# Kernel optimization log

Measured on AMD Instinct MI355X. Metric: run time of the kernel, lower is better.

## Reference

```python
import jax, jax.numpy as jnp
import numpy as np

B, T, H = 16, 1024, 256
L = 2048
NUM_CLASSES = 100000

def setup_inputs() -> dict:
    key = jax.random.key(0)
    k1, k2, k3 = jax.random.split(key, 3)
    inputs = jax.random.normal(k1, (B, T, H), dtype=jnp.float32)
    labels_selected = jax.random.randint(k2, (B, L), 0, NUM_CLASSES + 1, dtype=jnp.int64)
    attention_table = jax.random.normal(k3, (NUM_CLASSES + 1, H), dtype=jnp.float32) * 0.02
    return {"inputs": inputs, "labels_selected": labels_selected, "attention_table": attention_table}

def reference(inputs, labels_selected, attention_table):
    # Gather label embeddings as queries: (B, L, H)
    attn_weights = attention_table[labels_selected]
    # Unscaled dot-product scores: (B, L, T)
    scores = jnp.einsum('blh,bth->blt', attn_weights, inputs)
    attention = jax.nn.softmax(scores, axis=-1)
    # Weighted sum of inputs: (B, L, H)
    logits = jnp.einsum('blt,bth->blh', attention, inputs)
    return (logits, attention)
```

## Files before the change

kernel.cpp:

```cpp
#include <hip/hip_runtime.h>

#define Bdim 16
#define Tdim 1024
#define Hdim 256
#define Ldim 2048

typedef __attribute__((ext_vector_type(8))) short short8;
typedef __attribute__((ext_vector_type(4))) short short4_t;
typedef __attribute__((ext_vector_type(16))) float floatx16;

__device__ __forceinline__ ushort f2bf(float x) {
    union { float f; unsigned u; } v; v.f = x;
    unsigned r = v.u + 0x7fffu + ((v.u >> 16) & 1u);
    return (ushort)(r >> 16);
}
__device__ __forceinline__ float bf2f(ushort u) {
    union { unsigned u; float f; } v; v.u = ((unsigned)u) << 16;
    return v.f;
}
__device__ __forceinline__ short8 pack8(float4 a, float4 b) {
    short8 r;
    r[0] = (short)f2bf(a.x); r[1] = (short)f2bf(a.y); r[2] = (short)f2bf(a.z); r[3] = (short)f2bf(a.w);
    r[4] = (short)f2bf(b.x); r[5] = (short)f2bf(b.y); r[6] = (short)f2bf(b.z); r[7] = (short)f2bf(b.w);
    return r;
}

__global__ __launch_bounds__(256) void convert_kernel(
    const float* __restrict__ in, ushort* __restrict__ outN, ushort* __restrict__ outT) {
    __shared__ ushort lds[64][68];
    const int b = blockIdx.z, h0 = blockIdx.y * 64, t0 = blockIdx.x * 64;
    const int tid = threadIdx.x;
#pragma unroll
    for (int i = 0; i < 2; i++) {
        const int tt = tid + i * 256;
        const int r = tt >> 3, c = (tt & 7) * 8;
        const float4* src = (const float4*)(in + ((size_t)(b * Tdim + t0 + r)) * Hdim + h0 + c);
        short8 u = pack8(src[0], src[1]);
        *(short8*)(outN + ((size_t)(b * Tdim + t0 + r)) * Hdim + h0 + c) = u;
        short4_t lo = {u[0], u[1], u[2], u[3]}, hi = {u[4], u[5], u[6], u[7]};
        *(short4_t*)&lds[r][c] = lo;
        *(short4_t*)&lds[r][c + 4] = hi;
    }
    __syncthreads();
#pragma unroll
    for (int i = 0; i < 2; i++) {
        const int tt = tid + i * 256;
        const int hh = tt >> 3, c = (tt & 7) * 8;
        short8 u;
#pragma unroll
        for (int j = 0; j < 8; j++) u[j] = (short)lds[c + j][hh];
        *(short8*)(outT + ((size_t)(b * Hdim + h0 + hh)) * Tdim + t0 + c) = u;
    }
}

__global__ __launch_bounds__(512, 4) void attn_kernel(
    const float* __restrict__ table, const int* __restrict__ labels,
    const ushort* __restrict__ kn, const ushort* __restrict__ vt,
    float* __restrict__ logits_out, float* __restrict__ attn_out) {
    __shared__ ushort bufs[2][32][264];
    __shared__ float stats[8][32];
    float* rowinv = &stats[0][0];

    const int bid = blockIdx.x;
    const int xcd = bid & 7, w = bid >> 3;
    const int b = xcd * 2 + (w >> 6);
    const int l0 = (w & 63) * 32;
    const int tid = threadIdx.x;
    const int wave = tid >> 6, lane = tid & 63;
    const int half = lane >> 5, m = lane & 31;

    ushort (*qt)[264] = bufs[0];

    {
        const int row = tid >> 4, cc = (tid & 15) * 16;
        const int lab = labels[b * Ldim + l0 + row];
        const float4* src = (const float4*)(table + (size_t)lab * Hdim + cc);
        float4 f0 = src[0], f1 = src[1], f2 = src[2], f3 = src[3];
        *(short8*)&qt[row][cc] = pack8(f0, f1);
        *(short8*)&qt[row][cc + 8] = pack8(f2, f3);
    }
    __syncthreads();

    floatx16 acc[4];
#pragma unroll
    for (int nt = 0; nt < 4; nt++)
#pragma unroll
        for (int r = 0; r < 16; r++) acc[nt][r] = 0.f;
    {
        const int t0s = wave * 128;
        const ushort* kb = kn + ((size_t)(b * Tdim + t0s + m)) * Hdim + half * 8;
        const ushort* qb = &qt[m][half * 8];
#pragma unroll
        for (int ks = 0; ks < 16; ks++) {
            short8 af = *(const short8*)(qb + ks * 16);
            short8 b0 = *(const short8*)(kb + ks * 16);
            short8 b1 = *(const short8*)(kb + 32 * Hdim + ks * 16);
            short8 b2 = *(const short8*)(kb + 64 * Hdim + ks * 16);
            short8 b3 = *(const short8*)(kb + 96 * Hdim + ks * 16);
            acc[0] = __builtin_amdgcn_mfma_f32_32x32x16_bf16(af, b0, acc[0], 0, 0, 0);
            acc[1] = __builtin_amdgcn_mfma_f32_32x32x16_bf16(af, b1, acc[1], 0, 0, 0);
            acc[2] = __builtin_amdgcn_mfma_f32_32x32x16_bf16(af, b2, acc[2], 0, 0, 0);
            acc[3] = __builtin_amdgcn_mfma_f32_32x32x16_bf16(af, b3, acc[3], 0, 0, 0);
        }
    }

    float rs[16];
#pragma unroll
    for (int nt = 0; nt < 4; nt++)
#pragma unroll
        for (int r = 0; r < 16; r++) {
            float e = __expf(acc[nt][r]);
            acc[nt][r] = e;
            if (nt == 0) rs[r] = e; else rs[r] += e;
        }
#pragma unroll
    for (int s = 1; s < 32; s <<= 1)
#pragma unroll
        for (int r = 0; r < 16; r++) rs[r] += __shfl_xor(rs[r], s, 64);
    if (m == 0) {
#pragma unroll
        for (int r = 0; r < 16; r++) stats[wave][(r & 3) + 8 * (r >> 2) + 4 * half] = rs[r];
    }
    __syncthreads();

    if (tid < 32) {
        float d = 0.f;
#pragma unroll
        for (int wv = 0; wv < 8; wv++) d += stats[wv][tid];
        rowinv[tid] = 1.0f / d;
    }

    unsigned pk[2][16];
#pragma unroll
    for (int p = 0; p < 2; p++)
#pragma unroll
        for (int r = 0; r < 16; r++)
            pk[p][r] = (unsigned)f2bf(acc[2 * p][r]) |
                       ((unsigned)f2bf(acc[2 * p + 1][r]) << 16);

    const int coff = (wave & 1) * 128;
    auto write_strip = [&](int bi) {
        ushort(*dst)[264] = bufs[bi];
#pragma unroll
        for (int p = 0; p < 2; p++)
#pragma unroll
            for (int r = 0; r < 16; r++) {
                const int row = (r & 3) + 8 * (r >> 2) + 4 * half;
                dst[row][coff + (2 * p) * 32 + m] = (ushort)(pk[p][r] & 0xffffu);
                dst[row][coff + (2 * p + 1) * 32 + m] = (ushort)(pk[p][r] >> 16);
            }
    };

    if ((wave >> 1) == 0) write_strip(0);
    __syncthreads();

    {
        float inv[16];
#pragma unroll
        for (int r = 0; r < 16; r++) inv[r] = rowinv[(r & 3) + 8 * (r >> 2) + 4 * half];
        float* dst = attn_out + ((size_t)(b * Ldim + l0)) * Tdim + wave * 128 + m;
#pragma unroll
        for (int p = 0; p < 2; p++)
#pragma unroll
            for (int r = 0; r < 16; r++) {
                const int row = (r & 3) + 8 * (r >> 2) + 4 * half;
                dst[(size_t)row * Tdim + (2 * p) * 32] =
                    bf2f((ushort)(pk[p][r] & 0xffffu)) * inv[r];
                dst[(size_t)row * Tdim + (2 * p + 1) * 32] =
                    bf2f((ushort)(pk[p][r] >> 16)) * inv[r];
            }
    }

    {
        floatx16 c0, c1;
#pragma unroll
        for (int r = 0; r < 16; r++) { c0[r] = 0.f; c1[r] = 0.f; }
        const int h0 = wave * 32;
        const ushort* vb = vt + ((size_t)(b * Hdim + h0 + m)) * Tdim + half * 8;
#pragma unroll
        for (int c = 0; c < 4; c++) {
            if (c) __syncthreads();
            if (c < 3 && (wave >> 1) == c + 1) write_strip((c + 1) & 1);
            const ushort* pb = &bufs[c & 1][m][half * 8];
            const ushort* vc = vb + c * 256;
#pragma unroll
            for (int ks = 0; ks < 8; ks++) {
                short8 a0 = *(const short8*)(pb + (2 * ks) * 16);
                short8 v0 = *(const short8*)(vc + (2 * ks) * 16);
                c0 = __builtin_amdgcn_mfma_f32_32x32x16_bf16(a0, v0, c0, 0, 0, 0);
                short8 a1 = *(const short8*)(pb + (2 * ks + 1) * 16);
                short8 v1 = *(const short8*)(vc + (2 * ks + 1) * 16);
                c1 = __builtin_amdgcn_mfma_f32_32x32x16_bf16(a1, v1, c1, 0, 0, 0);
            }
        }
#pragma unroll
        for (int r = 0; r < 16; r++) {
            const int row = (r & 3) + 8 * (r >> 2) + 4 * half;
            logits_out[((size_t)(b * Ldim + l0 + row)) * Hdim + h0 + m] =
                (c0[r] + c1[r]) * rowinv[row];
        }
    }
}

extern "C" void kernel_launch(void* const* d_in, const int* in_sizes, int n_in,
                              void* d_out, int out_size, void* d_ws, size_t ws_size,
                              hipStream_t stream) {
    const float* inputs = (const float*)d_in[0];
    const int* labels   = (const int*)d_in[1];
    const float* table  = (const float*)d_in[2];
    float* out = (float*)d_out;

    ushort* kn = (ushort*)d_ws;
    ushort* vt = kn + (size_t)Bdim * Tdim * Hdim;

    convert_kernel<<<dim3(Tdim / 64, Hdim / 64, Bdim), 256, 0, stream>>>(inputs, kn, vt);

    float* logits_out = out;
    float* attn_out = out + (size_t)Bdim * Ldim * Hdim;
    attn_kernel<<<Bdim * (Ldim / 32), 512, 0, stream>>>(table, labels, kn, vt,
                                                        logits_out, attn_out);
}
```

Baseline: 350.5 us.

## Stage K and V tiles through LDS with async global-to-LDS double buffering

Replaces direct global loads of K and V fragments in both MFMA loops with buffer loads that write straight into per-wave LDS (global_load_lds). These are double-buffered and gated by explicit vmcnt/lgkmcnt waits so the next slice is fetched while the current one is multiplied. The Q and probability tiles move to XOR-swizzled LDS layouts to avoid bank conflicts, and the P·V phase is restructured into 8 smaller chunks. The intent is to hide global memory latency and get coalesced loads, at the cost of more barriers and hand-written wait counts that must match the issue order exactly.

```diff
diff --git a/kernel.cpp b/kernel.cpp
--- a/kernel.cpp
+++ b/kernel.cpp
@@ -24,6 +24,14 @@
     r[4] = (short)f2bf(b.x); r[5] = (short)f2bf(b.y); r[6] = (short)f2bf(b.z); r[7] = (short)f2bf(b.w);
     return r;
 }
+
+__device__ __forceinline__ void gload_lds16(const void* g, void* l) {
+    __builtin_amdgcn_global_load_lds((const __attribute__((address_space(1))) unsigned*)g,
+                                     (__attribute__((address_space(3))) unsigned*)l, 16, 0, 0);
+}
+#define VMCNT0() do { asm volatile("s_waitcnt vmcnt(0)" ::: "memory"); __builtin_amdgcn_sched_barrier(0); } while (0)
+#define VMCNT4() do { asm volatile("s_waitcnt vmcnt(4)" ::: "memory"); __builtin_amdgcn_sched_barrier(0); } while (0)
+#define LGKM0()  do { asm volatile("s_waitcnt lgkmcnt(0)" ::: "memory"); __builtin_amdgcn_sched_barrier(0); } while (0)
 
 __global__ __launch_bounds__(256) void convert_kernel(
     const float* __restrict__ in, ushort* __restrict__ outN, ushort* __restrict__ outT) {
@@ -57,9 +65,8 @@
     const float* __restrict__ table, const int* __restrict__ labels,
     const ushort* __restrict__ kn, const ushort* __restrict__ vt,
     float* __restrict__ logits_out, float* __restrict__ attn_out) {
-    __shared__ ushort bufs[2][32][264];
-    __shared__ float stats[8][32];
-    float* rowinv = &stats[0][0];
+    __shared__ ushort kst[8][2][2048];
+    __shared__ ushort P2[2][32][128];
 
     const int bid = blockIdx.x;
     const int xcd = bid & 7, w = bid >> 3;
@@ -69,16 +76,28 @@
     const int wave = tid >> 6, lane = tid & 63;
     const int half = lane >> 5, m = lane & 31;
 
-    ushort (*qt)[264] = bufs[0];
+    ushort (*qt)[256] = (ushort(*)[256]) & P2[0][0][0];
 
     {
-        const int row = tid >> 4, cc = (tid & 15) * 16;
+        const int row = tid >> 4, q16 = tid & 15;
         const int lab = labels[b * Ldim + l0 + row];
-        const float4* src = (const float4*)(table + (size_t)lab * Hdim + cc);
+        const float4* src = (const float4*)(table + (size_t)lab * Hdim + q16 * 16);
         float4 f0 = src[0], f1 = src[1], f2 = src[2], f3 = src[3];
-        *(short8*)&qt[row][cc] = pack8(f0, f1);
-        *(short8*)&qt[row][cc + 8] = pack8(f2, f3);
-    }
+        const int s0 = q16 * 2;
+        *(short8*)&qt[row][((s0) ^ (row & 15)) * 8] = pack8(f0, f1);
+        *(short8*)&qt[row][((s0 + 1) ^ (row & 15)) * 8] = pack8(f2, f3);
+    }
+
+    const int t0s = wave * 128;
+    const ushort* kbase[4];
+#pragma unroll
+    for (int j = 0; j < 4; j++)
+        kbase[j] = kn + ((size_t)(b * Tdim + t0s + j * 32 + (lane >> 1))) * Hdim + (lane & 1) * 8;
+#pragma unroll
+    for (int j = 0; j < 4; j++) gload_lds16(kbase[j], &kst[wave][0][j * 512]);
+#pragma unroll
+    for (int j = 0; j < 4; j++) gload_lds16(kbase[j] + 16, &kst[wave][1][j * 512]);
+
     __syncthreads();
 
     floatx16 acc[4];
@@ -86,21 +105,25 @@
     for (int nt = 0; nt < 4; nt++)
 #pragma unroll
         for (int r = 0; r < 16; r++) acc[nt][r] = 0.f;
-    {
-        const int t0s = wave * 128;
-        const ushort* kb = kn + ((size_t)(b * Tdim + t0s + m)) * Hdim + half * 8;
-        const ushort* qb = &qt[m][half * 8];
-#pragma unroll
-        for (int ks = 0; ks < 16; ks++) {
-            short8 af = *(const short8*)(qb + ks * 16);
-            short8 b0 = *(const short8*)(kb + ks * 16);
-            short8 b1 = *(const short8*)(kb + 32 * Hdim + ks * 16);
-            short8 b2 = *(const short8*)(kb + 64 * Hdim + ks * 16);
-            short8 b3 = *(const short8*)(kb + 96 * Hdim + ks * 16);
-            acc[0] = __builtin_amdgcn_mfma_f32_32x32x16_bf16(af, b0, acc[0], 0, 0, 0);
-            acc[1] = __builtin_amdgcn_mfma_f32_32x32x16_bf16(af, b1, acc[1], 0, 0, 0);
-            acc[2] = __builtin_amdgcn_mfma_f32_32x32x16_bf16(af, b2, acc[2], 0, 0, 0);
-            acc[3] = __builtin_amdgcn_mfma_f32_32x32x16_bf16(af, b3, acc[3], 0, 0, 0);
+#pragma unroll
+    for (int ks = 0; ks < 16; ks++) {
+        if (ks == 15) { VMCNT0(); }
+        else if (ks > 0) { VMCNT4(); }
+        const ushort* kw = &kst[wave][ks & 1][0];
+        short8 af = *(const short8*)&qt[m][(((ks * 2 + half)) ^ (m & 15)) * 8];
+        short8 b0 = *(const short8*)&kw[0 * 512 + (2 * m + half) * 8];
+        short8 b1 = *(const short8*)&kw[1 * 512 + (2 * m + half) * 8];
+        short8 b2 = *(const short8*)&kw[2 * 512 + (2 * m + half) * 8];
+        short8 b3 = *(const short8*)&kw[3 * 512 + (2 * m + half) * 8];
+        acc[0] = __builtin_amdgcn_mfma_f32_32x32x16_bf16(af, b0, acc[0], 0, 0, 0);
+        acc[1] = __builtin_amdgcn_mfma_f32_32x32x16_bf16(af, b1, acc[1], 0, 0, 0);
+        acc[2] = __builtin_amdgcn_mfma_f32_32x32x16_bf16(af, b2, acc[2], 0, 0, 0);
+        acc[3] = __builtin_amdgcn_mfma_f32_32x32x16_bf16(af, b3, acc[3], 0, 0, 0);
+        if (ks < 14) {
+            LGKM0();
+#pragma unroll
+            for (int j = 0; j < 4; j++)
+                gload_lds16(kbase[j] + (ks + 2) * 16, &kst[wave][ks & 1][j * 512]);
         }
     }
 
@@ -117,18 +140,25 @@
     for (int s = 1; s < 32; s <<= 1)
 #pragma unroll
         for (int r = 0; r < 16; r++) rs[r] += __shfl_xor(rs[r], s, 64);
+
+    float* sc = (float*)&P2[1][0][0];
+    float* rinv = sc + 256;
+    __syncthreads();
     if (m == 0) {
 #pragma unroll
-        for (int r = 0; r < 16; r++) stats[wave][(r & 3) + 8 * (r >> 2) + 4 * half] = rs[r];
-    }
-    __syncthreads();
-
+        for (int r = 0; r < 16; r++) sc[wave * 32 + (r & 3) + 8 * (r >> 2) + 4 * half] = rs[r];
+    }
+    __syncthreads();
     if (tid < 32) {
         float d = 0.f;
 #pragma unroll
-        for (int wv = 0; wv < 8; wv++) d += stats[wv][tid];
-        rowinv[tid] = 1.0f / d;
-    }
+        for (int wv = 0; wv < 8; wv++) d += sc[wv * 32 + tid];
+        rinv[tid] = 1.0f / d;
+    }
+    __syncthreads();
+    float inv[16];
+#pragma unroll
+    for (int r = 0; r < 16; r++) inv[r] = rinv[(r & 3) + 8 * (r >> 2) + 4 * half];
 
     unsigned pk[2][16];
 #pragma unroll
@@ -138,26 +168,23 @@
             pk[p][r] = (unsigned)f2bf(acc[2 * p][r]) |
                        ((unsigned)f2bf(acc[2 * p + 1][r]) << 16);
 
-    const int coff = (wave & 1) * 128;
     auto write_strip = [&](int bi) {
-        ushort(*dst)[264] = bufs[bi];
+        ushort* dst = &P2[bi][0][0];
 #pragma unroll
         for (int p = 0; p < 2; p++)
 #pragma unroll
             for (int r = 0; r < 16; r++) {
                 const int row = (r & 3) + 8 * (r >> 2) + 4 * half;
-                dst[row][coff + (2 * p) * 32 + m] = (ushort)(pk[p][r] & 0xffffu);
-                dst[row][coff + (2 * p + 1) * 32 + m] = (ushort)(pk[p][r] >> 16);
+                const int n0 = 2 * p, n1 = 2 * p + 1;
+                dst[row * 128 + (((n0 * 4 + (m >> 3)) ^ (row & 15)) * 8) + (m & 7)] =
+                    (ushort)(pk[p][r] & 0xffffu);
+                dst[row * 128 + (((n1 * 4 + (m >> 3)) ^ (row & 15)) * 8) + (m & 7)] =
+                    (ushort)(pk[p][r] >> 16);
             }
     };
-
-    if ((wave >> 1) == 0) write_strip(0);
-    __syncthreads();
+    if (wave == 0) write_strip(0);
 
     {
-        float inv[16];
-#pragma unroll
-        for (int r = 0; r < 16; r++) inv[r] = rowinv[(r & 3) + 8 * (r >> 2) + 4 * half];
         float* dst = attn_out + ((size_t)(b * Ldim + l0)) * Tdim + wave * 128 + m;
 #pragma unroll
         for (int p = 0; p < 2; p++)
@@ -171,34 +198,52 @@
             }
     }
 
-    {
-        floatx16 c0, c1;
-#pragma unroll
-        for (int r = 0; r < 16; r++) { c0[r] = 0.f; c1[r] = 0.f; }
-        const int h0 = wave * 32;
-        const ushort* vb = vt + ((size_t)(b * Hdim + h0 + m)) * Tdim + half * 8;
-#pragma unroll
-        for (int c = 0; c < 4; c++) {
-            if (c) __syncthreads();
-            if (c < 3 && (wave >> 1) == c + 1) write_strip((c + 1) & 1);
-            const ushort* pb = &bufs[c & 1][m][half * 8];
-            const ushort* vc = vb + c * 256;
-#pragma unroll
-            for (int ks = 0; ks < 8; ks++) {
-                short8 a0 = *(const short8*)(pb + (2 * ks) * 16);
-                short8 v0 = *(const short8*)(vc + (2 * ks) * 16);
-                c0 = __builtin_amdgcn_mfma_f32_32x32x16_bf16(a0, v0, c0, 0, 0, 0);
-                short8 a1 = *(const short8*)(pb + (2 * ks + 1) * 16);
-                short8 v1 = *(const short8*)(vc + (2 * ks + 1) * 16);
-                c1 = __builtin_amdgcn_mfma_f32_32x32x16_bf16(a1, v1, c1, 0, 0, 0);
-            }
-        }
-#pragma unroll
-        for (int r = 0; r < 16; r++) {
-            const int row = (r & 3) + 8 * (r >> 2) + 4 * half;
-            logits_out[((size_t)(b * Ldim + l0 + row)) * Hdim + h0 + m] =
-                (c0[r] + c1[r]) * rowinv[row];
-        }
+    const ushort* vbase = vt + ((size_t)(b * Hdim + wave * 32 + (lane >> 3))) * Tdim +
+                          ((lane & 7) ^ ((lane >> 3) & 7)) * 8;
+    auto issueV = [&](int vb, int tb) {
+#pragma unroll
+        for (int j = 0; j < 4; j++)
+            gload_lds16(vbase + (size_t)j * 8 * Tdim + tb, &kst[wave][vb][j * 512]);
+    };
+
+    issueV(0, 0);
+    __syncthreads();
+
+    floatx16 c0, c1;
+#pragma unroll
+    for (int r = 0; r < 16; r++) { c0[r] = 0.f; c1[r] = 0.f; }
+
+    for (int pc = 0; pc < 8; ++pc) {
+        if (pc) __syncthreads();
+        if (pc < 7 && wave == pc + 1) write_strip((pc + 1) & 1);
+        issueV(1, pc * 128 + 64);
+        const ushort* pw = &P2[pc & 1][0][0];
+        const ushort* vw0 = &kst[wave][0][0];
+        const ushort* vw1 = &kst[wave][1][0];
+#pragma unroll
+        for (int s = 0; s < 4; s++) {
+            short8 a = *(const short8*)&pw[m * 128 + (((s * 2 + half) ^ (m & 15)) * 8)];
+            short8 v = *(const short8*)&vw0[m * 64 + (((s * 2 + half) ^ (m & 7)) * 8)];
+            c0 = __builtin_amdgcn_mfma_f32_32x32x16_bf16(a, v, c0, 0, 0, 0);
+        }
+        VMCNT0();
+#pragma unroll
+        for (int s = 0; s < 4; s++) {
+            short8 a = *(const short8*)&pw[m * 128 + ((((s + 4) * 2 + half) ^ (m & 15)) * 8)];
+            short8 v = *(const short8*)&vw1[m * 64 + (((s * 2 + half) ^ (m & 7)) * 8)];
+            c1 = __builtin_amdgcn_mfma_f32_32x32x16_bf16(a, v, c1, 0, 0, 0);
+        }
+        if (pc < 7) {
+            LGKM0();
+            issueV(0, (pc + 1) * 128);
+        }
+    }
+
+#pragma unroll
+    for (int r = 0; r < 16; r++) {
+        const int row = (r & 3) + 8 * (r >> 2) + 4 * half;
+        logits_out[((size_t)(b * Ldim + l0 + row)) * Hdim + wave * 32 + m] =
+            (c0[r] + c1[r]) * inv[r];
     }
 }
 
```

New measurement: 686.7 us. 95.9% more time.
